# Kernel tuning notes

Measured on AMD Instinct MI355X. Metric: run time of the kernel, lower is better.

The kernel has to match this reference:

```python
import jax, jax.numpy as jnp
import numpy as np

H = 1024
E = 8
K = 2
N = 16384
LN_EPS = 1e-5


def _layernorm(h, g, b):
    m = jnp.mean(h, axis=-1, keepdims=True)
    v = jnp.mean(jnp.square(h - m), axis=-1, keepdims=True)
    return (h - m) * jax.lax.rsqrt(v + LN_EPS) * g + b


def setup_inputs() -> dict:
    key = jax.random.key(0)
    ks = jax.random.split(key, 8)
    s = 0.02
    return {
        "x": jax.random.normal(ks[0], (N, H), dtype=jnp.float32),
        "Wg": jax.random.normal(ks[1], (H, E), dtype=jnp.float32) * s,
        "bg": jnp.zeros((E,), dtype=jnp.float32),
        "W1": jax.random.normal(ks[2], (E, H, H), dtype=jnp.float32) * s,
        "b1": jnp.zeros((E, H), dtype=jnp.float32),
        "g1": jnp.ones((E, H), dtype=jnp.float32),
        "be1": jnp.zeros((E, H), dtype=jnp.float32),
        "W2": jax.random.normal(ks[3], (E, H, H), dtype=jnp.float32) * s,
        "b2": jnp.zeros((E, H), dtype=jnp.float32),
        "g2": jnp.ones((E, H), dtype=jnp.float32),
        "be2": jnp.zeros((E, H), dtype=jnp.float32),
    }


def reference(x, Wg, bg, W1, b1, g1, be1, W2, b2, g2, be2):
    # Gating: softmax over experts, top-k, renormalize
    gate_probs = jax.nn.softmax(x @ Wg + bg, axis=1)            # [N, E]
    tk_p, tk_i = jax.lax.top_k(gate_probs, K)                    # [N, K]
    tk_p = tk_p / (jnp.sum(tk_p, axis=1, keepdims=True) + 1e-9)
    # Dense per-expert combine weight (zero where expert not selected)
    w = jnp.sum(tk_p[:, :, None] * jax.nn.one_hot(tk_i, E, dtype=x.dtype), axis=1)  # [N, E]

    # ResidualBlock per expert, computed densely for all tokens (dropout = eval/no-op)
    h = jnp.einsum('nh,eho->eno', x, W1) + b1[:, None, :]        # [E, N, H]
    h = jax.nn.relu(_layernorm(h, g1[:, None, :], be1[:, None, :]))
    h = jnp.einsum('enh,eho->eno', h, W2) + b2[:, None, :]
    h = _layernorm(h, g2[:, None, :], be2[:, None, :])
    y = jax.nn.relu(x[None, :, :] + h)                           # [E, N, H]

    moe_out = jnp.einsum('ne,enh->nh', w, y)                     # [N, H]
    return moe_out, gate_probs
```

## Files before the change

kernel.cpp:

```cpp
#include <hip/hip_runtime.h>
#include <cstdint>
#include <cstddef>

constexpr int H_DIM = 1024;
constexpr int NE    = 8;
constexpr int NT    = 16384;
constexpr int NP    = NT * 2;

constexpr int BM = 128, BN = 128, BK = 32;
constexpr int NKT = H_DIM / BK;
constexpr int MAX_WG = (NP / BM + NE) * (H_DIM / BN);

typedef __attribute__((ext_vector_type(8)))  short          short8;
typedef __attribute__((ext_vector_type(8)))  unsigned short ushort8;
typedef __attribute__((ext_vector_type(4)))  float          f32x4;

__device__ __forceinline__ unsigned short f2bf(float f) {
  union { float f; uint32_t u; } c; c.f = f;
  uint32_t u = c.u;
  u = (u + 0x7fffu + ((u >> 16) & 1u)) >> 16;
  return (unsigned short)u;
}
__device__ __forceinline__ float bf2f(unsigned short h) {
  union { uint32_t u; float f; } c; c.u = ((uint32_t)h) << 16;
  return c.f;
}

__device__ __forceinline__ void gload16(const unsigned short* g, unsigned short* l) {
  __builtin_amdgcn_global_load_lds((const __attribute__((address_space(1))) void*)g,
                                   (__attribute__((address_space(3))) void*)l, 16, 0, 0);
}

__global__ __launch_bounds__(256) void prep_kernel(
    const float* __restrict__ X, const float* __restrict__ Wg,
    const float* __restrict__ bg, unsigned short* __restrict__ Xb,
    float* __restrict__ gate_out, int* __restrict__ tk_e, float* __restrict__ tk_w,
    const float* __restrict__ W1, const float* __restrict__ W2,
    unsigned short* __restrict__ T1, unsigned short* __restrict__ T2)
{
  __shared__ float tile[64][65];
  int b = blockIdx.x;
  if (b >= 4096) {
    int t = b - 4096;
    int zi = t >> 8;
    const float* W = (zi < 8) ? W1 : W2;
    unsigned short* T = (zi < 8) ? T1 : T2;
    int e  = zi & 7;
    int o0 = ((t >> 4) & 15) * 64;
    int h0 = (t & 15) * 64;
    int c  = threadIdx.x & 63;
    int r0 = (threadIdx.x >> 6) * 16;
    const float* src = W + ((size_t)e * H_DIM + h0) * H_DIM + o0;
#pragma unroll
    for (int i = 0; i < 16; ++i)
      tile[r0 + i][c] = src[(size_t)(r0 + i) * H_DIM + c];
    __syncthreads();
    unsigned short* dst = T + ((size_t)e * H_DIM + o0) * H_DIM + h0;
#pragma unroll
    for (int i = 0; i < 16; ++i)
      dst[(size_t)(r0 + i) * H_DIM + c] = f2bf(tile[c][r0 + i]);
    return;
  }

  int wid = threadIdx.x >> 6, lane = threadIdx.x & 63;
  int n = b * 4 + wid;
  const float* xr = X + (size_t)n * H_DIM;

  const float4* xp = (const float4*)(xr + lane * 16);
  float4 f0 = xp[0], f1 = xp[1], f2 = xp[2], f3 = xp[3];
  float v[16] = {f0.x,f0.y,f0.z,f0.w, f1.x,f1.y,f1.z,f1.w,
                 f2.x,f2.y,f2.z,f2.w, f3.x,f3.y,f3.z,f3.w};

  ushort8 u0, u1;
#pragma unroll
  for (int j = 0; j < 8; ++j) { u0[j] = f2bf(v[j]); u1[j] = f2bf(v[8 + j]); }
  ushort8* xb = (ushort8*)(Xb + (size_t)n * H_DIM + lane * 16);
  xb[0] = u0; xb[1] = u1;

  float acc[8];
#pragma unroll
  for (int e = 0; e < 8; ++e) acc[e] = 0.f;
#pragma unroll
  for (int j = 0; j < 16; ++j) {
    int h = lane * 16 + j;
    const float4* wg = (const float4*)(Wg + (size_t)h * 8);
    float4 a = wg[0], bb = wg[1];
    float xv = v[j];
    acc[0] += xv * a.x;  acc[1] += xv * a.y;  acc[2] += xv * a.z;  acc[3] += xv * a.w;
    acc[4] += xv * bb.x; acc[5] += xv * bb.y; acc[6] += xv * bb.z; acc[7] += xv * bb.w;
  }
#pragma unroll
  for (int m = 1; m < 64; m <<= 1) {
#pragma unroll
    for (int e = 0; e < 8; ++e) acc[e] += __shfl_xor(acc[e], m);
  }
#pragma unroll
  for (int e = 0; e < 8; ++e) acc[e] += bg[e];

  float mx = acc[0];
#pragma unroll
  for (int e = 1; e < 8; ++e) mx = fmaxf(mx, acc[e]);
  float g[8], s = 0.f;
#pragma unroll
  for (int e = 0; e < 8; ++e) { g[e] = __expf(acc[e] - mx); s += g[e]; }
  float inv = 1.f / s;
#pragma unroll
  for (int e = 0; e < 8; ++e) g[e] *= inv;

  int e0 = 0; float b0 = g[0];
#pragma unroll
  for (int e = 1; e < 8; ++e) if (g[e] > b0) { b0 = g[e]; e0 = e; }
  int e1 = -1; float b1v = -1.f;
#pragma unroll
  for (int e = 0; e < 8; ++e) if (e != e0 && g[e] > b1v) { b1v = g[e]; e1 = e; }
  float s2 = b0 + b1v + 1e-9f;

  if (lane == 0) {
    float4* gp = (float4*)(gate_out + (size_t)n * 8);
    gp[0] = make_float4(g[0], g[1], g[2], g[3]);
    gp[1] = make_float4(g[4], g[5], g[6], g[7]);
    tk_e[2 * n] = e0; tk_e[2 * n + 1] = e1;
    tk_w[2 * n] = b0 / s2; tk_w[2 * n + 1] = b1v / s2;
  }
}

__global__ __launch_bounds__(256) void hist_kernel(
    const int* __restrict__ tk_e, int* __restrict__ blockHist)
{
  __shared__ int h[8];
  if (threadIdx.x < 8) h[threadIdx.x] = 0;
  __syncthreads();
  int i0 = blockIdx.x * 512 + threadIdx.x;
  atomicAdd(&h[tk_e[i0]], 1);
  atomicAdd(&h[tk_e[i0 + 256]], 1);
  __syncthreads();
  if (threadIdx.x < 8) blockHist[blockIdx.x * 8 + threadIdx.x] = h[threadIdx.x];
}

__global__ void scan_worklist_kernel(const int* __restrict__ blockHist,
                                     int* __restrict__ blockBase,
                                     int* __restrict__ count, int* __restrict__ offs,
                                     int* __restrict__ wl, int* __restrict__ wlCount)
{
  __shared__ int nmt[8], ebase[8], totalS;
  int e = threadIdx.x;
  if (e < 8) {
    int run = 0;
    for (int b = 0; b < 64; ++b) { blockBase[b * 8 + e] = run; run += blockHist[b * 8 + e]; }
    count[e] = run;
  }
  __syncthreads();
  if (threadIdx.x == 0) {
    int o = 0, wo = 0;
    for (int k = 0; k < 8; ++k) {
      offs[k] = o; o += count[k];
      nmt[k] = (count[k] + BM - 1) / BM;
      ebase[k] = wo; wo += nmt[k] * (H_DIM / BN);
    }
    totalS = wo; wlCount[0] = wo;
  }
  __syncthreads();
  if (e < 8) {
    int o = offs[e];
    for (int b = 0; b < 64; ++b) blockBase[b * 8 + e] += o;
  }
  int total = totalS;
  for (int i = threadIdx.x; i < total; i += blockDim.x) {
    int ee = 0;
    while (ee < 7 && i >= ebase[ee + 1]) ++ee;
    int loc = i - ebase[ee];
    int nt = loc / nmt[ee];
    int mt = loc - nt * nmt[ee];
    wl[i] = (ee << 20) | (nt << 16) | mt;
  }
}

__global__ __launch_bounds__(256) void place_kernel(
    const int* __restrict__ tk_e, const int* __restrict__ blockBase,
    int* __restrict__ pairTok, int* __restrict__ pairExp, int* __restrict__ slots)
{
  __shared__ int cur[8];
  if (threadIdx.x < 8) cur[threadIdx.x] = blockBase[blockIdx.x * 8 + threadIdx.x];
  __syncthreads();
#pragma unroll
  for (int j = 0; j < 2; ++j) {
    int i = blockIdx.x * 512 + j * 256 + threadIdx.x;
    int e = tk_e[i];
    int s = atomicAdd(&cur[e], 1);
    pairTok[s] = i >> 1; pairExp[s] = e; slots[i] = s;
  }
}

template<bool GATHER>
__global__ __launch_bounds__(256, 3) void gemm4d_kernel(
    const unsigned short* __restrict__ Ab,
    const unsigned short* __restrict__ Bt,
    const float* __restrict__ bias,
    const int* __restrict__ pairTok,
    const int* __restrict__ count, const int* __restrict__ offs,
    const int* __restrict__ wl, const int* __restrict__ wlCount,
    unsigned short* __restrict__ Out)
{
  __shared__ unsigned short As[4 * 4096];
  __shared__ unsigned short Bs[4 * 4096];

  const int total = wlCount[0];
  const int orig = blockIdx.x;
  if (orig >= total) return;
  const int qq = total >> 3, rr = total & 7;
  const int xcd = orig & 7, sub = orig >> 3;
  const int idx = (xcd < rr ? xcd * (qq + 1) : rr * (qq + 1) + (xcd - rr) * qq) + sub;
  const int ent = wl[idx];
  const int e = ent >> 20, ntb = (ent >> 16) & 15, mtb = ent & 0xffff;
  const int cnt = count[e], base = offs[e];

  const int tid = threadIdx.x;
  const int wid = tid >> 6, l = tid & 63;
  const int wr = wid >> 1, wc = wid & 1;

  const int rsub = (l >> 2);
  const int kswz = ((l & 3) * 8) ^ (((l >> 5) & 1) << 4);

  const unsigned short *apg0, *apg1, *bpg0, *bpg1;
  {
    int r0 = wid * 16 + rsub;
    int r1 = 64 + wid * 16 + rsub;
    int g0 = mtb * BM + r0; if (g0 >= cnt) g0 = cnt - 1;
    int g1 = mtb * BM + r1; if (g1 >= cnt) g1 = cnt - 1;
    size_t a0, a1;
    if (GATHER) { a0 = (size_t)pairTok[base + g0]; a1 = (size_t)pairTok[base + g1]; }
    else        { a0 = (size_t)(base + g0);        a1 = (size_t)(base + g1); }
    apg0 = Ab + a0 * H_DIM + kswz;
    apg1 = Ab + a1 * H_DIM + kswz;
    const unsigned short* bb = Bt + ((size_t)e * H_DIM + ntb * BN) * H_DIM + kswz;
    bpg0 = bb + (size_t)r0 * H_DIM;
    bpg1 = bb + (size_t)r1 * H_DIM;
  }

  const int loff = ((l & 15) * 64 + (l >> 4) * 16) ^ (((l >> 3) & 1) << 5);

  auto STAGE = [&](int u, int slot) {
    unsigned short* ad = As + slot * 4096 + wid * 512;
    unsigned short* bd = Bs + slot * 4096 + wid * 512;
    gload16(apg0 + (size_t)u * BK, ad);
    gload16(apg1 + (size_t)u * BK, ad + 2048);
    gload16(bpg0 + (size_t)u * BK, bd);
    gload16(bpg1 + (size_t)u * BK, bd + 2048);
  };

  STAGE(0, 0); STAGE(1, 1); STAGE(2, 2);
  asm volatile("s_waitcnt vmcnt(8)" ::: "memory");
  __builtin_amdgcn_s_barrier();

  f32x4 acc[4][4] = {};

#pragma unroll 4
  for (int t = 0; t < NKT; ++t) {
    const int sl = t & 3;
    const char* aB = (const char*)As + sl * 8192 + wr * 4096 + loff;
    const char* bB = (const char*)Bs + sl * 8192 + wc * 4096 + loff;

    short8 af[4], bfr[4];
#pragma unroll
    for (int j = 0; j < 4; ++j) af[j] = *(const short8*)(aB + j * 1024);
#pragma unroll
    for (int r = 0; r < 4; ++r) bfr[r] = *(const short8*)(bB + r * 1024);

    if (t + 3 < NKT) STAGE(t + 3, (t + 3) & 3);

    __builtin_amdgcn_s_setprio(1);
#pragma unroll
    for (int j = 0; j < 4; ++j)
#pragma unroll
      for (int r = 0; r < 4; ++r)
        acc[j][r] = __builtin_amdgcn_mfma_f32_16x16x32_bf16(af[j], bfr[r], acc[j][r], 0, 0, 0);
    __builtin_amdgcn_s_setprio(0);

    if (t + 3 < NKT)       asm volatile("s_waitcnt vmcnt(8)" ::: "memory");
    else if (t + 3 == NKT) asm volatile("s_waitcnt vmcnt(4)" ::: "memory");
    else if (t + 2 == NKT) asm volatile("s_waitcnt vmcnt(0)" ::: "memory");
    __builtin_amdgcn_s_barrier();
  }

  float bvv[4];
#pragma unroll
  for (int r = 0; r < 4; ++r)
    bvv[r] = bias[e * H_DIM + ntb * BN + wc * 64 + r * 16 + (l & 15)];
#pragma unroll
  for (int j = 0; j < 4; ++j) {
    int grow0 = mtb * BM + wr * 64 + j * 16 + (l >> 4) * 4;
#pragma unroll
    for (int r = 0; r < 4; ++r) {
      int gcol = ntb * BN + wc * 64 + r * 16 + (l & 15);
#pragma unroll
      for (int v = 0; v < 4; ++v) {
        int row = grow0 + v;
        if (row < cnt)
          Out[(size_t)(base + row) * H_DIM + gcol] = f2bf(acc[j][r][v] + bvv[r]);
      }
    }
  }
}

__global__ __launch_bounds__(256) void ln_relu_kernel(
    unsigned short* __restrict__ buf, const float* __restrict__ gamma,
    const float* __restrict__ beta, const int* __restrict__ pairExp)
{
  int wid = threadIdx.x >> 6, lane = threadIdx.x & 63;
  int row = blockIdx.x * 4 + wid;
  int e = pairExp[row];
  unsigned short* r = buf + (size_t)row * H_DIM;
  ushort8 u0 = ((const ushort8*)r)[lane];
  ushort8 u1 = ((const ushort8*)r)[lane + 64];
  float v[16];
#pragma unroll
  for (int j = 0; j < 8; ++j) { v[j] = bf2f(u0[j]); v[8 + j] = bf2f(u1[j]); }
  float s = 0.f, ss = 0.f;
#pragma unroll
  for (int j = 0; j < 16; ++j) { s += v[j]; ss += v[j] * v[j]; }
#pragma unroll
  for (int m = 1; m < 64; m <<= 1) { s += __shfl_xor(s, m); ss += __shfl_xor(ss, m); }
  float mean = s * (1.f / 1024.f);
  float var  = ss * (1.f / 1024.f) - mean * mean;
  float rs   = rsqrtf(var + 1e-5f);

  int h0 = lane * 8, h1 = 512 + lane * 8;
  const float4* gp0 = (const float4*)(gamma + (size_t)e * H_DIM + h0);
  const float4* bp0 = (const float4*)(beta  + (size_t)e * H_DIM + h0);
  const float4* gp1 = (const float4*)(gamma + (size_t)e * H_DIM + h1);
  const float4* bp1 = (const float4*)(beta  + (size_t)e * H_DIM + h1);
  float4 ga = gp0[0], gb = gp0[1], gc = gp1[0], gd = gp1[1];
  float4 ba = bp0[0], bb = bp0[1], bc = bp1[0], bd = bp1[1];
  float gv[16] = {ga.x,ga.y,ga.z,ga.w, gb.x,gb.y,gb.z,gb.w,
                  gc.x,gc.y,gc.z,gc.w, gd.x,gd.y,gd.z,gd.w};
  float bv[16] = {ba.x,ba.y,ba.z,ba.w, bb.x,bb.y,bb.z,bb.w,
                  bc.x,bc.y,bc.z,bc.w, bd.x,bd.y,bd.z,bd.w};
#pragma unroll
  for (int j = 0; j < 8; ++j) {
    float t0 = fmaxf((v[j]     - mean) * rs * gv[j]     + bv[j],     0.f);
    float t1 = fmaxf((v[8 + j] - mean) * rs * gv[8 + j] + bv[8 + j], 0.f);
    u0[j] = f2bf(t0); u1[j] = f2bf(t1);
  }
  ((ushort8*)r)[lane] = u0; ((ushort8*)r)[lane + 64] = u1;
}

__global__ __launch_bounds__(256) void combine_kernel(
    const unsigned short* __restrict__ buf2, const float* __restrict__ X,
    const float* __restrict__ g2, const float* __restrict__ be2,
    const int* __restrict__ slots, const int* __restrict__ tk_e,
    const float* __restrict__ tk_w, float* __restrict__ out)
{
  int wid = threadIdx.x >> 6, lane = threadIdx.x & 63;
  int n = blockIdx.x * 4 + wid;
  int h0 = lane * 8, h1 = 512 + lane * 8;

  const float4* xp0 = (const float4*)(X + (size_t)n * H_DIM + h0);
  const float4* xp1 = (const float4*)(X + (size_t)n * H_DIM + h1);
  float4 xa = xp0[0], xb = xp0[1], xc = xp1[0], xd = xp1[1];
  float xv[16] = {xa.x,xa.y,xa.z,xa.w, xb.x,xb.y,xb.z,xb.w,
                  xc.x,xc.y,xc.z,xc.w, xd.x,xd.y,xd.z,xd.w};
  float o[16];
#pragma unroll
  for (int j = 0; j < 16; ++j) o[j] = 0.f;

#pragma unroll
  for (int k = 0; k < 2; ++k) {
    int slot = slots[2 * n + k];
    int e = tk_e[2 * n + k];
    float w = tk_w[2 * n + k];
    const unsigned short* r = buf2 + (size_t)slot * H_DIM;
    ushort8 u0 = ((const ushort8*)r)[lane];
    ushort8 u1 = ((const ushort8*)r)[lane + 64];
    float v[16];
#pragma unroll
    for (int j = 0; j < 8; ++j) { v[j] = bf2f(u0[j]); v[8 + j] = bf2f(u1[j]); }
    float s = 0.f, ss = 0.f;
#pragma unroll
    for (int j = 0; j < 16; ++j) { s += v[j]; ss += v[j] * v[j]; }
#pragma unroll
    for (int m = 1; m < 64; m <<= 1) { s += __shfl_xor(s, m); ss += __shfl_xor(ss, m); }
    float mean = s * (1.f / 1024.f);
    float var  = ss * (1.f / 1024.f) - mean * mean;
    float rs   = rsqrtf(var + 1e-5f);

    const float4* gp0 = (const float4*)(g2  + (size_t)e * H_DIM + h0);
    const float4* bp0 = (const float4*)(be2 + (size_t)e * H_DIM + h0);
    const float4* gp1 = (const float4*)(g2  + (size_t)e * H_DIM + h1);
    const float4* bp1 = (const float4*)(be2 + (size_t)e * H_DIM + h1);
    float4 ga = gp0[0], gb = gp0[1], gc = gp1[0], gd = gp1[1];
    float4 ba = bp0[0], bb = bp0[1], bc = bp1[0], bd = bp1[1];
    float gv[16] = {ga.x,ga.y,ga.z,ga.w, gb.x,gb.y,gb.z,gb.w,
                    gc.x,gc.y,gc.z,gc.w, gd.x,gd.y,gd.z,gd.w};
    float bvv[16] = {ba.x,ba.y,ba.z,ba.w, bb.x,bb.y,bb.z,bb.w,
                     bc.x,bc.y,bc.z,bc.w, bd.x,bd.y,bd.z,bd.w};
#pragma unroll
    for (int j = 0; j < 16; ++j) {
      float u = (v[j] - mean) * rs * gv[j] + bvv[j];
      float y = fmaxf(xv[j] + u, 0.f);
      o[j] += w * y;
    }
  }

  float4* op0 = (float4*)(out + (size_t)n * H_DIM + h0);
  float4* op1 = (float4*)(out + (size_t)n * H_DIM + h1);
  op0[0] = make_float4(o[0], o[1], o[2], o[3]);
  op0[1] = make_float4(o[4], o[5], o[6], o[7]);
  op1[0] = make_float4(o[8], o[9], o[10], o[11]);
  op1[1] = make_float4(o[12], o[13], o[14], o[15]);
}

extern "C" void kernel_launch(void* const* d_in, const int* in_sizes, int n_in,
                              void* d_out, int out_size, void* d_ws, size_t ws_size,
                              hipStream_t stream)
{
  const float* x   = (const float*)d_in[0];
  const float* Wg  = (const float*)d_in[1];
  const float* bg  = (const float*)d_in[2];
  const float* W1  = (const float*)d_in[3];
  const float* b1  = (const float*)d_in[4];
  const float* g1  = (const float*)d_in[5];
  const float* be1 = (const float*)d_in[6];
  const float* W2  = (const float*)d_in[7];
  const float* b2  = (const float*)d_in[8];
  const float* g2  = (const float*)d_in[9];
  const float* be2 = (const float*)d_in[10];
  float* out = (float*)d_out;
  float* gate_out = out + (size_t)NT * H_DIM;

  char* ws = (char*)d_ws;
  size_t off = 0;
  auto alloc = [&](size_t bytes) { char* p = ws + off; off += (bytes + 255) & ~(size_t)255; return p; };
  unsigned short* w1bt = (unsigned short*)alloc((size_t)NE * H_DIM * H_DIM * 2);
  unsigned short* w2bt = (unsigned short*)alloc((size_t)NE * H_DIM * H_DIM * 2);
  unsigned short* buf1 = (unsigned short*)alloc((size_t)NP * H_DIM * 2);
  unsigned short* buf2 = (unsigned short*)alloc((size_t)NP * H_DIM * 2);
  int*   tk_e      = (int*)alloc((size_t)NP * 4);
  float* tk_w      = (float*)alloc((size_t)NP * 4);
  int*   pairTok   = (int*)alloc((size_t)NP * 4);
  int*   pairExp   = (int*)alloc((size_t)NP * 4);
  int*   slots     = (int*)alloc((size_t)NP * 4);
  int*   blockHist = (int*)alloc(64 * 8 * 4);
  int*   blockBase = (int*)alloc(64 * 8 * 4);
  int*   count     = (int*)alloc(8 * 4);
  int*   offs      = (int*)alloc(8 * 4);
  int*   wl        = (int*)alloc(MAX_WG * 4);
  int*   wlCount   = (int*)alloc(4);
  (void)in_sizes; (void)n_in; (void)out_size; (void)ws_size;

  unsigned short* Xb = buf2;

  prep_kernel<<<dim3(8192), 256, 0, stream>>>(
      x, Wg, bg, Xb, gate_out, tk_e, tk_w, W1, W2, w1bt, w2bt);
  hist_kernel<<<dim3(64), 256, 0, stream>>>(tk_e, blockHist);
  scan_worklist_kernel<<<dim3(1), 256, 0, stream>>>(
      blockHist, blockBase, count, offs, wl, wlCount);
  place_kernel<<<dim3(64), 256, 0, stream>>>(tk_e, blockBase, pairTok, pairExp, slots);
  gemm4d_kernel<true><<<dim3(MAX_WG), 256, 0, stream>>>(
      Xb, w1bt, b1, pairTok, count, offs, wl, wlCount, buf1);
  ln_relu_kernel<<<dim3(NP / 4), 256, 0, stream>>>(buf1, g1, be1, pairExp);
  gemm4d_kernel<false><<<dim3(MAX_WG), 256, 0, stream>>>(
      buf1, w2bt, b2, pairTok, count, offs, wl, wlCount, buf2);
  combine_kernel<<<dim3(NT / 4), 256, 0, stream>>>(
      buf2, x, g2, be2, slots, tk_e, tk_w, out);
}
```

Measured before the change: 430.3 us.

## Widen grouped GEMM tile to 256x128 with 3-stage pipeline and 1x4 warp layout

Doubles the M tile of the grouped expert GEMMs to 256 rows, with each of the four waves owning a 64x128 sub-tile (4x8 MFMA accumulators). The shared-memory pipeline drops from four stages to three so the larger A tile fits, and occupancy is lowered to two blocks per CU. The goal is more MFMA work per LDS fragment load and fewer reloads of expert weights across row tiles. In exchange, register pressure rises, pipelining depth falls, and padding waste on the last tile of each expert grows.

After: 414.2 us. 3.8% less time.

```diff
diff --git a/kernel.cpp b/kernel.cpp
--- a/kernel.cpp
+++ b/kernel.cpp
@@ -7,7 +7,7 @@
 constexpr int NT    = 16384;
 constexpr int NP    = NT * 2;
 
-constexpr int BM = 128, BN = 128, BK = 32;
+constexpr int BM = 256, BN = 128, BK = 32;
 constexpr int NKT = H_DIM / BK;
 constexpr int MAX_WG = (NP / BM + NE) * (H_DIM / BN);
 
@@ -192,7 +192,7 @@
 }
 
 template<bool GATHER>
-__global__ __launch_bounds__(256, 3) void gemm4d_kernel(
+__global__ __launch_bounds__(256, 2) void gemmw_kernel(
     const unsigned short* __restrict__ Ab,
     const unsigned short* __restrict__ Bt,
     const float* __restrict__ bias,
@@ -201,8 +201,8 @@
     const int* __restrict__ wl, const int* __restrict__ wlCount,
     unsigned short* __restrict__ Out)
 {
-  __shared__ unsigned short As[4 * 4096];
-  __shared__ unsigned short Bs[4 * 4096];
+  __shared__ unsigned short As[3 * 8192];
+  __shared__ unsigned short Bs[3 * 4096];
 
   const int total = wlCount[0];
   const int orig = blockIdx.x;
@@ -216,82 +216,83 @@
 
   const int tid = threadIdx.x;
   const int wid = tid >> 6, l = tid & 63;
-  const int wr = wid >> 1, wc = wid & 1;
 
   const int rsub = (l >> 2);
   const int kswz = ((l & 3) * 8) ^ (((l >> 5) & 1) << 4);
 
-  const unsigned short *apg0, *apg1, *bpg0, *bpg1;
-  {
-    int r0 = wid * 16 + rsub;
-    int r1 = 64 + wid * 16 + rsub;
-    int g0 = mtb * BM + r0; if (g0 >= cnt) g0 = cnt - 1;
-    int g1 = mtb * BM + r1; if (g1 >= cnt) g1 = cnt - 1;
-    size_t a0, a1;
-    if (GATHER) { a0 = (size_t)pairTok[base + g0]; a1 = (size_t)pairTok[base + g1]; }
-    else        { a0 = (size_t)(base + g0);        a1 = (size_t)(base + g1); }
-    apg0 = Ab + a0 * H_DIM + kswz;
-    apg1 = Ab + a1 * H_DIM + kswz;
-    const unsigned short* bb = Bt + ((size_t)e * H_DIM + ntb * BN) * H_DIM + kswz;
-    bpg0 = bb + (size_t)r0 * H_DIM;
-    bpg1 = bb + (size_t)r1 * H_DIM;
+  const unsigned short* apg[4];
+#pragma unroll
+  for (int j = 0; j < 4; ++j) {
+    int g = mtb * BM + (j * 4 + wid) * 16 + rsub;
+    if (g >= cnt) g = cnt - 1;
+    size_t arow = GATHER ? (size_t)pairTok[base + g] : (size_t)(base + g);
+    apg[j] = Ab + arow * H_DIM + kswz;
+  }
+  const unsigned short* bpg[2];
+#pragma unroll
+  for (int j = 0; j < 2; ++j) {
+    int col = ntb * BN + (j * 4 + wid) * 16 + rsub;
+    bpg[j] = Bt + ((size_t)e * H_DIM + col) * H_DIM + kswz;
   }
 
   const int loff = ((l & 15) * 64 + (l >> 4) * 16) ^ (((l >> 3) & 1) << 5);
 
   auto STAGE = [&](int u, int slot) {
-    unsigned short* ad = As + slot * 4096 + wid * 512;
+    unsigned short* ad = As + slot * 8192 + wid * 512;
     unsigned short* bd = Bs + slot * 4096 + wid * 512;
-    gload16(apg0 + (size_t)u * BK, ad);
-    gload16(apg1 + (size_t)u * BK, ad + 2048);
-    gload16(bpg0 + (size_t)u * BK, bd);
-    gload16(bpg1 + (size_t)u * BK, bd + 2048);
+#pragma unroll
+    for (int j = 0; j < 4; ++j)
+      gload16(apg[j] + (size_t)u * BK, ad + j * 2048);
+#pragma unroll
+    for (int j = 0; j < 2; ++j)
+      gload16(bpg[j] + (size_t)u * BK, bd + j * 2048);
   };
 
-  STAGE(0, 0); STAGE(1, 1); STAGE(2, 2);
-  asm volatile("s_waitcnt vmcnt(8)" ::: "memory");
+  STAGE(0, 0); STAGE(1, 1);
+  asm volatile("s_waitcnt vmcnt(6)" ::: "memory");
   __builtin_amdgcn_s_barrier();
 
-  f32x4 acc[4][4] = {};
-
-#pragma unroll 4
+  f32x4 acc[4][8] = {};
+
+  int sl = 0, sstage = 2;
   for (int t = 0; t < NKT; ++t) {
-    const int sl = t & 3;
-    const char* aB = (const char*)As + sl * 8192 + wr * 4096 + loff;
-    const char* bB = (const char*)Bs + sl * 8192 + wc * 4096 + loff;
-
-    short8 af[4], bfr[4];
+    const char* aB = (const char*)As + sl * 16384 + wid * 4096 + loff;
+    const char* bB = (const char*)Bs + sl * 8192 + loff;
+
+    short8 af[4], bfr[8];
 #pragma unroll
     for (int j = 0; j < 4; ++j) af[j] = *(const short8*)(aB + j * 1024);
 #pragma unroll
-    for (int r = 0; r < 4; ++r) bfr[r] = *(const short8*)(bB + r * 1024);
-
-    if (t + 3 < NKT) STAGE(t + 3, (t + 3) & 3);
+    for (int r = 0; r < 8; ++r) bfr[r] = *(const short8*)(bB + r * 1024);
+
+    if (t + 2 < NKT) STAGE(t + 2, sstage);
 
     __builtin_amdgcn_s_setprio(1);
 #pragma unroll
     for (int j = 0; j < 4; ++j)
 #pragma unroll
-      for (int r = 0; r < 4; ++r)
+      for (int r = 0; r < 8; ++r)
         acc[j][r] = __builtin_amdgcn_mfma_f32_16x16x32_bf16(af[j], bfr[r], acc[j][r], 0, 0, 0);
     __builtin_amdgcn_s_setprio(0);
 
-    if (t + 3 < NKT)       asm volatile("s_waitcnt vmcnt(8)" ::: "memory");
-    else if (t + 3 == NKT) asm volatile("s_waitcnt vmcnt(4)" ::: "memory");
+    if (t + 2 < NKT)       asm volatile("s_waitcnt vmcnt(6)" ::: "memory");
     else if (t + 2 == NKT) asm volatile("s_waitcnt vmcnt(0)" ::: "memory");
     __builtin_amdgcn_s_barrier();
-  }
-
-  float bvv[4];
-#pragma unroll
-  for (int r = 0; r < 4; ++r)
-    bvv[r] = bias[e * H_DIM + ntb * BN + wc * 64 + r * 16 + (l & 15)];
+
+    sl = (sl == 2) ? 0 : sl + 1;
+    sstage = (sstage == 2) ? 0 : sstage + 1;
+  }
+
+  float bvv[8];
+#pragma unroll
+  for (int r = 0; r < 8; ++r)
+    bvv[r] = bias[e * H_DIM + ntb * BN + r * 16 + (l & 15)];
 #pragma unroll
   for (int j = 0; j < 4; ++j) {
-    int grow0 = mtb * BM + wr * 64 + j * 16 + (l >> 4) * 4;
-#pragma unroll
-    for (int r = 0; r < 4; ++r) {
-      int gcol = ntb * BN + wc * 64 + r * 16 + (l & 15);
+    int grow0 = mtb * BM + wid * 64 + j * 16 + (l >> 4) * 4;
+#pragma unroll
+    for (int r = 0; r < 8; ++r) {
+      int gcol = ntb * BN + r * 16 + (l & 15);
 #pragma unroll
       for (int v = 0; v < 4; ++v) {
         int row = grow0 + v;
@@ -455,10 +456,10 @@
   scan_worklist_kernel<<<dim3(1), 256, 0, stream>>>(
       blockHist, blockBase, count, offs, wl, wlCount);
   place_kernel<<<dim3(64), 256, 0, stream>>>(tk_e, blockBase, pairTok, pairExp, slots);
-  gemm4d_kernel<true><<<dim3(MAX_WG), 256, 0, stream>>>(
+  gemmw_kernel<true><<<dim3(MAX_WG), 256, 0, stream>>>(
       Xb, w1bt, b1, pairTok, count, offs, wl, wlCount, buf1);
   ln_relu_kernel<<<dim3(NP / 4), 256, 0, stream>>>(buf1, g1, be1, pairExp);
-  gemm4d_kernel<false><<<dim3(MAX_WG), 256, 0, stream>>>(
+  gemmw_kernel<false><<<dim3(MAX_WG), 256, 0, stream>>>(
       buf1, w2bt, b2, pairTok, count, offs, wl, wlCount, buf2);
   combine_kernel<<<dim3(NT / 4), 256, 0, stream>>>(
       buf2, x, g2, be2, slots, tk_e, tk_w, out);
```
